# Optimization experiments

Hardware: AMD Instinct MI355X
Metric: run time of the kernel (lower is better)

## Reference

```python
import jax, jax.numpy as jnp
import numpy as np

D_MODEL = 1024
D_FF = 4096
EPS = 1e-6


def _rms_norm(x, eps=EPS):
    var = jnp.mean(x * x, axis=-1, keepdims=True) + eps
    return x * jax.lax.rsqrt(var)


def setup_inputs() -> dict:
    key = jax.random.key(0)
    kx, kw = jax.random.split(key)
    x = jax.random.normal(kx, (4, 4096, D_MODEL), dtype=jnp.float32)
    std = np.sqrt(2.0 / (D_FF + D_MODEL))
    # trunc_normal_(mean=0, std, a=-3std, b=3std) approximated by clipped normal
    w = jax.random.truncated_normal(kw, -3.0, 3.0, (D_FF, D_MODEL), dtype=jnp.float32) * std
    return {"x": x, "weight": w}


def reference(x, weight):
    # scores: [..., d_ff] = rmsnorm(x) @ rmsnorm(weight).T
    scores = jnp.einsum('bsd,cd->bsc', _rms_norm(x), _rms_norm(weight))
    probs = jax.nn.softmax(scores, axis=-1)
    return jnp.einsum('bsc,cd->bsd', probs, weight)
```

## Files before the change

kernel.cpp:

```cpp
#include <hip/hip_runtime.h>
#include <hip/hip_fp16.h>


#define D_MODEL 1024
#define D_FF    4096
#define M_ROWS  16384
#define MC      4096

typedef _Float16 half8 __attribute__((ext_vector_type(8)));
typedef _Float16 half4 __attribute__((ext_vector_type(4)));
typedef float    floatx4 __attribute__((ext_vector_type(4)));

__device__ __forceinline__ void gld_lds16(const void* g, void* l) {
  __builtin_amdgcn_global_load_lds(
      (const __attribute__((address_space(1))) void*)g,
      (__attribute__((address_space(3))) void*)l, 16, 0, 0);
}

#define MB_X (M_ROWS / 4)
#define MB_W (D_FF / 4)
__global__ __launch_bounds__(256) void rmsnorm_split_kernel(
    const float* __restrict__ X, _Float16* __restrict__ XH,
    _Float16* __restrict__ XL, const float* __restrict__ W,
    _Float16* __restrict__ WH, _Float16* __restrict__ WL) {
  const int lane = threadIdx.x & 63;
  const bool isW = blockIdx.x >= MB_X;
  const long row = (long)(isW ? blockIdx.x - MB_X : blockIdx.x) * 4 +
                   (threadIdx.x >> 6);
  const float* x = (isW ? W : X) + row * D_MODEL;
  _Float16* YH = (isW ? WH : XH) + row * D_MODEL;
  _Float16* YL = (isW ? WL : XL) + row * D_MODEL;

  float v[16];
  float ss = 0.f;
#pragma unroll
  for (int s = 0; s < 4; s++) {
    const float4 f = *(const float4*)(x + s * 256 + lane * 4);
    v[s * 4 + 0] = f.x; v[s * 4 + 1] = f.y;
    v[s * 4 + 2] = f.z; v[s * 4 + 3] = f.w;
    ss += f.x * f.x + f.y * f.y + f.z * f.z + f.w * f.w;
  }
#pragma unroll
  for (int off = 32; off >= 1; off >>= 1) ss += __shfl_xor(ss, off);
  const float inv = rsqrtf(ss * (1.0f / D_MODEL) + 1e-6f);
#pragma unroll
  for (int s = 0; s < 4; s++) {
    half4 h, l;
#pragma unroll
    for (int j = 0; j < 4; j++) {
      const float t = v[s * 4 + j] * inv;
      const _Float16 hi = (_Float16)t;
      h[j] = hi;
      l[j] = (_Float16)(t - (float)hi);
    }
    *(half4*)(YH + s * 256 + lane * 4) = h;
    *(half4*)(YL + s * 256 + lane * 4) = l;
  }
}

__global__ __launch_bounds__(256) void transpose_kernel(
    const float* __restrict__ W, _Float16* __restrict__ WT) {
  __shared__ _Float16 tile[32][33];
  const int tx = threadIdx.x & 31;
  const int ty = threadIdx.x >> 5;
  const int d0 = blockIdx.x * 32;
  const int c0 = blockIdx.y * 32;
#pragma unroll
  for (int i = 0; i < 32; i += 8)
    tile[ty + i][tx] = (_Float16)W[(long)(c0 + ty + i) * D_MODEL + d0 + tx];
  __syncthreads();
#pragma unroll
  for (int i = 0; i < 32; i += 8)
    WT[(long)(d0 + ty + i) * D_FF + c0 + tx] = tile[tx][ty + i];
}


__global__ __launch_bounds__(256, 2) void gemm1_kernel(
    const _Float16* __restrict__ XH, const _Float16* __restrict__ XL,
    const _Float16* __restrict__ WH, float* __restrict__ S) {
  constexpr int BK = 64;
  __shared__ _Float16 Ah[128 * BK];
  __shared__ _Float16 Al[128 * BK];
  __shared__ _Float16 Bs[256 * BK];
  const int tid = threadIdx.x;
  const int wave = tid >> 6, lane = tid & 63;
  const long rowBase = (long)blockIdx.y * 128;
  const long colBase = (long)blockIdx.x * 256;
  const int srow = lane >> 3;
  const int scol = ((lane & 7) ^ (lane >> 3)) * 8;
  const _Float16* AgH = XH + (rowBase + wave * 32 + srow) * (long)D_MODEL + scol;
  const _Float16* AgL = XL + (rowBase + wave * 32 + srow) * (long)D_MODEL + scol;
  const _Float16* Bg  = WH + (colBase + wave * 64 + srow) * (long)D_MODEL + scol;
  const int ldsOffA = wave * 2048 + lane * 8;
  const int ldsOffB = wave * 4096 + lane * 8;
  const int wr = wave >> 1, wc = wave & 1;
  const int m16 = lane & 15, q = lane >> 4;
  const int mx7 = m16 & 7;

  floatx4 acc[4][8] = {};

  for (int kt = 0; kt < D_MODEL; kt += BK) {
#pragma unroll
    for (int i = 0; i < 4; i++) {
      gld_lds16(AgH + i * 8 * D_MODEL + kt, Ah + ldsOffA + i * 512);
      gld_lds16(AgL + i * 8 * D_MODEL + kt, Al + ldsOffA + i * 512);
    }
#pragma unroll
    for (int i = 0; i < 8; i++)
      gld_lds16(Bg + i * 8 * D_MODEL + kt, Bs + ldsOffB + i * 512);
    __syncthreads();
#pragma unroll
    for (int ks = 0; ks < 2; ks++) {
      const int kx = ((ks * 4 + q) ^ mx7) * 8;
      half8 b[8], a[4];
#pragma unroll
      for (int ni = 0; ni < 8; ni++)
        b[ni] = *(const half8*)(&Bs[(wc * 128 + ni * 16 + m16) * BK + kx]);
#pragma unroll
      for (int mi = 0; mi < 4; mi++)
        a[mi] = *(const half8*)(&Ah[(wr * 64 + mi * 16 + m16) * BK + kx]);
#pragma unroll
      for (int mi = 0; mi < 4; mi++)
#pragma unroll
        for (int ni = 0; ni < 8; ni++)
          acc[mi][ni] = __builtin_amdgcn_mfma_f32_16x16x32_f16(
              a[mi], b[ni], acc[mi][ni], 0, 0, 0);
#pragma unroll
      for (int mi = 0; mi < 4; mi++)
        a[mi] = *(const half8*)(&Al[(wr * 64 + mi * 16 + m16) * BK + kx]);
#pragma unroll
      for (int mi = 0; mi < 4; mi++)
#pragma unroll
        for (int ni = 0; ni < 8; ni++)
          acc[mi][ni] = __builtin_amdgcn_mfma_f32_16x16x32_f16(
              a[mi], b[ni], acc[mi][ni], 0, 0, 0);
    }
    __syncthreads();
  }

#pragma unroll
  for (int mi = 0; mi < 4; mi++)
#pragma unroll
    for (int r = 0; r < 4; r++) {
      const long rr = rowBase + wr * 64 + mi * 16 + q * 4 + r;
#pragma unroll
      for (int ni = 0; ni < 8; ni++)
        S[rr * D_FF + colBase + wc * 128 + ni * 16 + m16] = acc[mi][ni][r];
    }
}

__global__ __launch_bounds__(256, 2) void gemm2_kernel(
    const _Float16* __restrict__ P, const _Float16* __restrict__ WT,
    float* __restrict__ O) {
  constexpr int BK = 128, K = D_FF, LDA = 2 * D_FF, KSPLIT = 2048;
  __shared__ _Float16 As[128 * BK];
  __shared__ _Float16 Bs[128 * BK];
  const int tid = threadIdx.x;
  const int wave = tid >> 6, lane = tid & 63;

  const int bid = ((blockIdx.z * 32 + blockIdx.y) << 3) | blockIdx.x;
  const int swz = ((bid & 7) << 6) | (bid >> 3);
  const int bx = swz & 7;
  const int by = (swz >> 3) & 31;
  const int bz = swz >> 8;

  const long rowBase = (long)by * 128;
  const long colBase = (long)bx * 128;
  const int k0 = bz * KSPLIT;

  const int srow4 = lane >> 4;
  const int slotE = (lane & 15) ^ srow4;
  const int slotO = slotE ^ 4;
  const _Float16* AgE = P + (rowBase + wave * 32 + srow4) * (long)LDA + slotE * 8;
  const _Float16* AgO = P + (rowBase + wave * 32 + srow4) * (long)LDA + slotO * 8;
  const _Float16* BgE = WT + (colBase + wave * 32 + srow4) * (long)K + slotE * 8;
  const _Float16* BgO = WT + (colBase + wave * 32 + srow4) * (long)K + slotO * 8;
  _Float16* AsW = As + wave * 4096 + lane * 8;
  _Float16* BsW = Bs + wave * 4096 + lane * 8;
  const int wr = wave >> 1, wc = wave & 1;
  const int m16 = lane & 15, q = lane >> 4;
  const int mx7 = m16 & 7;

  floatx4 acc[4][4] = {};

  for (int kt = k0; kt < k0 + KSPLIT; kt += BK) {
#pragma unroll
    for (int i = 0; i < 8; i++) {
      const _Float16* ag = (i & 1) ? AgO : AgE;
      const _Float16* bg = (i & 1) ? BgO : BgE;
      gld_lds16(ag + (long)i * 4 * LDA + kt, AsW + i * 512);
      gld_lds16(bg + (long)i * 4 * K + kt, BsW + i * 512);
    }
    __syncthreads();
#pragma unroll
    for (int ks = 0; ks < 4; ks++) {
      const int kx = ((ks * 4 + q) ^ mx7) * 8;
      half8 a[4], b[4];
#pragma unroll
      for (int mi = 0; mi < 4; mi++)
        a[mi] = *(const half8*)(&As[(wr * 64 + mi * 16 + m16) * BK + kx]);
#pragma unroll
      for (int ni = 0; ni < 4; ni++)
        b[ni] = *(const half8*)(&Bs[(wc * 64 + ni * 16 + m16) * BK + kx]);
#pragma unroll
      for (int mi = 0; mi < 4; mi++)
#pragma unroll
        for (int ni = 0; ni < 4; ni++)
          acc[mi][ni] = __builtin_amdgcn_mfma_f32_16x16x32_f16(
              a[mi], b[ni], acc[mi][ni], 0, 0, 0);
    }
    __syncthreads();
  }

#pragma unroll
  for (int mi = 0; mi < 4; mi++)
#pragma unroll
    for (int r = 0; r < 4; r++) {
      const long rr = rowBase + wr * 64 + mi * 16 + q * 4 + r;
#pragma unroll
      for (int ni = 0; ni < 4; ni++)
        unsafeAtomicAdd(&O[rr * D_MODEL + colBase + wc * 64 + ni * 16 + m16],
                        acc[mi][ni][r]);
    }
}

__global__ __launch_bounds__(256) void softmax_kernel(float* __restrict__ S) {
  float* s = S + (long)blockIdx.x * D_FF;
  const int t = threadIdx.x;
  const int lane = t & 63, wave = t >> 6;
  __shared__ float redm[4], redl[4];

  float v[16];
  float mx = -3.4e38f;
#pragma unroll
  for (int seg = 0; seg < 4; seg++) {
    const float4 f = *(const float4*)(s + seg * 1024 + t * 4);
    v[seg * 4 + 0] = f.x; v[seg * 4 + 1] = f.y;
    v[seg * 4 + 2] = f.z; v[seg * 4 + 3] = f.w;
  }
#pragma unroll
  for (int j = 0; j < 16; j++) mx = fmaxf(mx, v[j]);
#pragma unroll
  for (int off = 32; off >= 1; off >>= 1) mx = fmaxf(mx, __shfl_xor(mx, off));
  if (lane == 0) redm[wave] = mx;
  __syncthreads();
  const float m = fmaxf(fmaxf(redm[0], redm[1]), fmaxf(redm[2], redm[3]));

  float sum = 0.f;
#pragma unroll
  for (int j = 0; j < 16; j++) {
    v[j] = __expf(v[j] - m);
    sum += v[j];
  }
#pragma unroll
  for (int off = 32; off >= 1; off >>= 1) sum += __shfl_xor(sum, off);
  if (lane == 0) redl[wave] = sum;
  __syncthreads();
  const float inv = 1.f / (redl[0] + redl[1] + redl[2] + redl[3]);

  _Float16* p = (_Float16*)s;
#pragma unroll
  for (int seg = 0; seg < 4; seg++) {
    half4 h;
#pragma unroll
    for (int j = 0; j < 4; j++) h[j] = (_Float16)(v[seg * 4 + j] * inv);
    *(half4*)(p + seg * 1024 + t * 4) = h;
  }
}

extern "C" void kernel_launch(void* const* d_in, const int* in_sizes, int n_in,
                              void* d_out, int out_size, void* d_ws, size_t ws_size,
                              hipStream_t stream) {
  const float* x = (const float*)d_in[0];
  const float* w = (const float*)d_in[1];
  float* out = (float*)d_out;

  const size_t NEED = 152ull << 20;
  if (ws_size < NEED) return;

  char* ws = (char*)d_ws;
  _Float16* xh = (_Float16*)(ws);
  _Float16* xl = (_Float16*)(ws + (32ull << 20));
  _Float16* wh = (_Float16*)(ws + (64ull << 20));
  _Float16* wl = (_Float16*)(ws + (72ull << 20));
  _Float16* wT = (_Float16*)(ws + (80ull << 20));
  float*    S  = (float*)   (ws + (88ull << 20));

  hipMemsetAsync(d_out, 0, (size_t)M_ROWS * D_MODEL * sizeof(float), stream);

  hipLaunchKernelGGL(rmsnorm_split_kernel, dim3(MB_X + MB_W), dim3(256), 0,
                     stream, x, xh, xl, w, wh, wl);
  hipLaunchKernelGGL(transpose_kernel, dim3(D_MODEL / 32, D_FF / 32), dim3(256),
                     0, stream, w, wT);

  for (int c = 0; c < M_ROWS / MC; c++) {
    const long ro = (long)c * MC;
    hipLaunchKernelGGL(gemm1_kernel, dim3(D_FF / 256, MC / 128), dim3(256), 0,
                       stream, xh + ro * D_MODEL, xl + ro * D_MODEL, wh, S);
    hipLaunchKernelGGL(softmax_kernel, dim3(MC), dim3(256), 0, stream, S);
    hipLaunchKernelGGL(gemm2_kernel, dim3(D_MODEL / 128, MC / 128, 2),
                       dim3(256), 0, stream, (const _Float16*)S, wT,
                       out + ro * D_MODEL);
  }
}
```

Before: 650.3 us.

## Double-buffer gemm1 with 512 threads, interleaved async loads and block swizzle

Rewrites the first GEMM (scores = XH/XL × WH) to use 8 waves per block and double-buffered LDS, so global-to-LDS loads for the next K tile are issued between MFMA phases, with explicit vmcnt/lgkmcnt waits and setprio. It also swizzles the block index to improve L2 reuse of the W tiles. The goal is to hide global load latency that the previous single-buffer loop exposed at every K step. In exchange, LDS use doubles to about 128 KB per block, which may limit occupancy, and the hand-placed waitcnt and barrier schedule is fragile.

```diff
diff --git a/kernel.cpp b/kernel.cpp
--- a/kernel.cpp
+++ b/kernel.cpp
@@ -74,69 +74,127 @@
     WT[(long)(d0 + ty + i) * D_FF + c0 + tx] = tile[tx][ty + i];
 }
 
-
-__global__ __launch_bounds__(256, 2) void gemm1_kernel(
+__global__ __launch_bounds__(512, 2) void gemm1_kernel(
     const _Float16* __restrict__ XH, const _Float16* __restrict__ XL,
     const _Float16* __restrict__ WH, float* __restrict__ S) {
-  constexpr int BK = 64;
-  __shared__ _Float16 Ah[128 * BK];
-  __shared__ _Float16 Al[128 * BK];
-  __shared__ _Float16 Bs[256 * BK];
+  __shared__ _Float16 Bs[2][256 * 64];
+  __shared__ _Float16 Ah[2][128 * 64];
+  __shared__ _Float16 Al[2][128 * 64];
   const int tid = threadIdx.x;
-  const int wave = tid >> 6, lane = tid & 63;
-  const long rowBase = (long)blockIdx.y * 128;
-  const long colBase = (long)blockIdx.x * 256;
-  const int srow = lane >> 3;
-  const int scol = ((lane & 7) ^ (lane >> 3)) * 8;
-  const _Float16* AgH = XH + (rowBase + wave * 32 + srow) * (long)D_MODEL + scol;
-  const _Float16* AgL = XL + (rowBase + wave * 32 + srow) * (long)D_MODEL + scol;
-  const _Float16* Bg  = WH + (colBase + wave * 64 + srow) * (long)D_MODEL + scol;
-  const int ldsOffA = wave * 2048 + lane * 8;
-  const int ldsOffB = wave * 4096 + lane * 8;
-  const int wr = wave >> 1, wc = wave & 1;
-  const int m16 = lane & 15, q = lane >> 4;
-  const int mx7 = m16 & 7;
-
-  floatx4 acc[4][8] = {};
-
-  for (int kt = 0; kt < D_MODEL; kt += BK) {
-#pragma unroll
-    for (int i = 0; i < 4; i++) {
-      gld_lds16(AgH + i * 8 * D_MODEL + kt, Ah + ldsOffA + i * 512);
-      gld_lds16(AgL + i * 8 * D_MODEL + kt, Al + ldsOffA + i * 512);
-    }
-#pragma unroll
-    for (int i = 0; i < 8; i++)
-      gld_lds16(Bg + i * 8 * D_MODEL + kt, Bs + ldsOffB + i * 512);
-    __syncthreads();
-#pragma unroll
-    for (int ks = 0; ks < 2; ks++) {
-      const int kx = ((ks * 4 + q) ^ mx7) * 8;
-      half8 b[8], a[4];
-#pragma unroll
-      for (int ni = 0; ni < 8; ni++)
-        b[ni] = *(const half8*)(&Bs[(wc * 128 + ni * 16 + m16) * BK + kx]);
-#pragma unroll
-      for (int mi = 0; mi < 4; mi++)
-        a[mi] = *(const half8*)(&Ah[(wr * 64 + mi * 16 + m16) * BK + kx]);
-#pragma unroll
-      for (int mi = 0; mi < 4; mi++)
-#pragma unroll
-        for (int ni = 0; ni < 8; ni++)
-          acc[mi][ni] = __builtin_amdgcn_mfma_f32_16x16x32_f16(
-              a[mi], b[ni], acc[mi][ni], 0, 0, 0);
-#pragma unroll
-      for (int mi = 0; mi < 4; mi++)
-        a[mi] = *(const half8*)(&Al[(wr * 64 + mi * 16 + m16) * BK + kx]);
-#pragma unroll
-      for (int mi = 0; mi < 4; mi++)
-#pragma unroll
-        for (int ni = 0; ni < 8; ni++)
-          acc[mi][ni] = __builtin_amdgcn_mfma_f32_16x16x32_f16(
-              a[mi], b[ni], acc[mi][ni], 0, 0, 0);
-    }
-    __syncthreads();
-  }
+  const int lane = tid & 63;
+  const int wave = tid >> 6;
+
+  const int bid = blockIdx.y * 16 + blockIdx.x;
+  const int swz = ((bid & 7) << 6) | (bid >> 3);
+  const int bx = swz & 15, by = swz >> 4;
+  const long rowBase = (long)by * 128;
+  const long colBase = (long)bx * 256;
+
+  const int srow = tid >> 3;
+  const int scol = ((tid & 7) ^ (srow & 7)) * 8;
+  const _Float16* Bg  = WH + (colBase + srow) * (long)D_MODEL + scol;
+  const _Float16* Ahg = XH + (rowBase + srow) * (long)D_MODEL + scol;
+  const _Float16* Alg = XL + (rowBase + srow) * (long)D_MODEL + scol;
+  const int dstOff = tid * 8;
+
+  const int wr = wave >> 2, wc = wave & 3;
+  const int m16 = lane & 15, q = lane >> 4, mx7 = m16 & 7;
+  const int aRow = wr * 64, bRow = wc * 64;
+
+  floatx4 acc[4][4] = {};
+  half8 b0[4], b1[4], a[4];
+
+#define RD_A4(buf, ksl)                                                        \
+  _Pragma("unroll") for (int mi = 0; mi < 4; mi++) a[mi] =                     \
+      *(const half8*)(&buf[(aRow + mi * 16 + m16) * 64 +                       \
+                           (((ksl)*4 + q) ^ mx7) * 8]);
+#define RD_B4(buf, dst, ksl)                                                   \
+  _Pragma("unroll") for (int ni = 0; ni < 4; ni++) dst[ni] =                   \
+      *(const half8*)(&buf[(bRow + ni * 16 + m16) * 64 +                       \
+                           (((ksl)*4 + q) ^ mx7) * 8]);
+#define MFMA16(BF)                                                             \
+  __builtin_amdgcn_s_setprio(1);                                               \
+  _Pragma("unroll") for (int mi = 0; mi < 4; mi++)                             \
+  _Pragma("unroll") for (int ni = 0; ni < 4; ni++)                             \
+      acc[mi][ni] = __builtin_amdgcn_mfma_f32_16x16x32_f16(                    \
+          a[mi], BF[ni], acc[mi][ni], 0, 0, 0);                                \
+  __builtin_amdgcn_s_setprio(0);
+#define BAR() __builtin_amdgcn_s_barrier()
+#define LGKM0() asm volatile("s_waitcnt lgkmcnt(0)" ::: "memory")
+
+  {
+#pragma unroll
+    for (int r = 0; r < 4; r++)
+      gld_lds16(Bg + (long)r * 64 * D_MODEL, &Bs[0][r * 4096 + dstOff]);
+#pragma unroll
+    for (int r = 0; r < 2; r++)
+      gld_lds16(Ahg + (long)r * 64 * D_MODEL, &Ah[0][r * 4096 + dstOff]);
+#pragma unroll
+    for (int r = 0; r < 2; r++)
+      gld_lds16(Alg + (long)r * 64 * D_MODEL, &Al[0][r * 4096 + dstOff]);
+    asm volatile("s_waitcnt vmcnt(2)" ::: "memory");
+    BAR();
+    __builtin_amdgcn_sched_barrier(0);
+  }
+
+  for (int i = 0; i < 16; i++) {
+    const int cur = i & 1, nxt = cur ^ 1;
+    const long ktn = (long)(i + 1) * 64;
+    const bool lastI = (i == 15);
+
+    RD_B4(Bs[cur], b0, 0);
+    RD_A4(Ah[cur], 0);
+    if (!lastI) {
+      gld_lds16(Bg + (long)0 * 64 * D_MODEL + ktn, &Bs[nxt][0 * 4096 + dstOff]);
+      gld_lds16(Bg + (long)1 * 64 * D_MODEL + ktn, &Bs[nxt][1 * 4096 + dstOff]);
+    }
+    BAR();
+    LGKM0();
+    MFMA16(b0);
+    BAR();
+
+    RD_B4(Bs[cur], b1, 1);
+    RD_A4(Ah[cur], 1);
+    if (!lastI) {
+      gld_lds16(Bg + (long)2 * 64 * D_MODEL + ktn, &Bs[nxt][2 * 4096 + dstOff]);
+      gld_lds16(Bg + (long)3 * 64 * D_MODEL + ktn, &Bs[nxt][3 * 4096 + dstOff]);
+      asm volatile("s_waitcnt vmcnt(4)" ::: "memory");
+    } else {
+      asm volatile("s_waitcnt vmcnt(0)" ::: "memory");
+    }
+    BAR();
+    LGKM0();
+    MFMA16(b1);
+    BAR();
+    __builtin_amdgcn_sched_barrier(0);
+
+    RD_A4(Al[cur], 0);
+    if (!lastI) {
+      gld_lds16(Ahg + (long)0 * 64 * D_MODEL + ktn, &Ah[nxt][0 * 4096 + dstOff]);
+      gld_lds16(Ahg + (long)1 * 64 * D_MODEL + ktn, &Ah[nxt][1 * 4096 + dstOff]);
+    }
+    BAR();
+    LGKM0();
+    MFMA16(b0);
+    BAR();
+
+    RD_A4(Al[cur], 1);
+    if (!lastI) {
+      gld_lds16(Alg + (long)0 * 64 * D_MODEL + ktn, &Al[nxt][0 * 4096 + dstOff]);
+      gld_lds16(Alg + (long)1 * 64 * D_MODEL + ktn, &Al[nxt][1 * 4096 + dstOff]);
+      asm volatile("s_waitcnt vmcnt(2)" ::: "memory");
+    }
+    BAR();
+    LGKM0();
+    MFMA16(b1);
+    BAR();
+    __builtin_amdgcn_sched_barrier(0);
+  }
+#undef RD_A4
+#undef RD_B4
+#undef MFMA16
+#undef BAR
+#undef LGKM0
 
 #pragma unroll
   for (int mi = 0; mi < 4; mi++)
@@ -144,8 +202,8 @@
     for (int r = 0; r < 4; r++) {
       const long rr = rowBase + wr * 64 + mi * 16 + q * 4 + r;
 #pragma unroll
-      for (int ni = 0; ni < 8; ni++)
-        S[rr * D_FF + colBase + wc * 128 + ni * 16 + m16] = acc[mi][ni][r];
+      for (int ni = 0; ni < 4; ni++)
+        S[rr * D_FF + colBase + wc * 64 + ni * 16 + m16] = acc[mi][ni][r];
     }
 }
 
@@ -295,7 +353,7 @@
 
   for (int c = 0; c < M_ROWS / MC; c++) {
     const long ro = (long)c * MC;
-    hipLaunchKernelGGL(gemm1_kernel, dim3(D_FF / 256, MC / 128), dim3(256), 0,
+    hipLaunchKernelGGL(gemm1_kernel, dim3(D_FF / 256, MC / 128), dim3(512), 0,
                        stream, xh + ro * D_MODEL, xl + ro * D_MODEL, wh, S);
     hipLaunchKernelGGL(softmax_kernel, dim3(MC), dim3(256), 0, stream, S);
     hipLaunchKernelGGL(gemm2_kernel, dim3(D_MODEL / 128, MC / 128, 2),
```

Measured after the change: 665.2 us. 2.3% more time.
